# Kernel optimization log

Hardware: AMD Instinct MI355X
Metric: run time of the kernel (lower is better)

The kernel has to match this reference:

```python
import jax, jax.numpy as jnp
import numpy as np

NUM_HEADS = 32
NUM_KV_HEADS = 8
HEAD_DIM = 128
ROPE_BASE = 10000.0


def _rope_tables(seq_len, head_dim, dtype):
    inv_freq = 1.0 / (ROPE_BASE ** (jnp.arange(0, head_dim, 2, dtype=jnp.float32) / head_dim))
    t = jnp.arange(seq_len, dtype=jnp.float32)
    freqs = jnp.einsum('i,j->ij', t, inv_freq)          # [S, D/2]
    emb = jnp.concatenate([freqs, freqs], axis=-1)      # [S, D]
    return jnp.cos(emb).astype(dtype), jnp.sin(emb).astype(dtype)


def _rotate_half(x):
    x1, x2 = jnp.split(x, 2, axis=-1)
    return jnp.concatenate([-x2, x1], axis=-1)


def _apply_rope(x, cos, sin):
    # x: [B, H, S, D]; cos/sin: [S, D] broadcast over batch and heads
    return x * cos[None, None, :, :] + _rotate_half(x) * sin[None, None, :, :]


def setup_inputs() -> dict:
    key = jax.random.key(0)
    k1, k2, k3, k4, k5 = jax.random.split(key, 5)
    B, S, H = 1, 2048, 4096
    scale = 0.02
    return {
        'hidden_states': jax.random.normal(k1, (B, S, H), dtype=jnp.float32),
        'Wq': jax.random.normal(k2, (4096, 4096), dtype=jnp.float32) * scale,
        'Wk': jax.random.normal(k3, (1024, 4096), dtype=jnp.float32) * scale,
        'Wv': jax.random.normal(k4, (1024, 4096), dtype=jnp.float32) * scale,
        'Wo': jax.random.normal(k5, (4096, 4096), dtype=jnp.float32) * scale,
    }


def reference(hidden_states, Wq, Wk, Wv, Wo):
    B, S, hidden = hidden_states.shape
    n_rep = NUM_HEADS // NUM_KV_HEADS

    # projections (torch Linear: y = x @ W.T)
    q = (hidden_states @ Wq.T).reshape(B, S, NUM_HEADS, HEAD_DIM).transpose(0, 2, 1, 3)
    k = (hidden_states @ Wk.T).reshape(B, S, NUM_KV_HEADS, HEAD_DIM).transpose(0, 2, 1, 3)
    v = (hidden_states @ Wv.T).reshape(B, S, NUM_KV_HEADS, HEAD_DIM).transpose(0, 2, 1, 3)

    # RoPE: init path with no past -> query/key position ids both arange(S)
    cos, sin = _rope_tables(S, HEAD_DIM, hidden_states.dtype)
    q = _apply_rope(q, cos, sin)
    k = _apply_rope(k, cos, sin)

    # repeat_kv: [B, Hkv, S, D] -> [B, H, S, D]
    k = jnp.repeat(k, n_rep, axis=1)
    v = jnp.repeat(v, n_rep, axis=1)

    # manual attention with causal mask
    scores = jnp.einsum('bhqd,bhkd->bhqk', q, k) / jnp.sqrt(jnp.float32(HEAD_DIM)).astype(q.dtype)
    causal = jnp.tril(jnp.ones((S, S), dtype=bool))
    scores = jnp.where(causal[None, None, :, :], scores, jnp.finfo(scores.dtype).min)
    probs = jax.nn.softmax(scores, axis=-1)

    out = jnp.einsum('bhqk,bhkd->bhqd', probs, v)        # [B, H, S, D]
    out = out.transpose(0, 2, 1, 3).reshape(B, S, hidden)
    return out @ Wo.T
```

## Files before the change

kernel.cpp:

```cpp
#include <hip/hip_runtime.h>
#include <hip/hip_bf16.h>

typedef __attribute__((ext_vector_type(4))) float f32x4;
typedef __attribute__((ext_vector_type(8))) short short8;
typedef __attribute__((ext_vector_type(4))) unsigned int u32x4;

__device__ __forceinline__ unsigned short f2bf(float f) {
  union { float f; unsigned int u; } v; v.f = f;
  unsigned int r = (v.u + 0x7fffu + ((v.u >> 16) & 1u)) >> 16;
  return (unsigned short)r;
}
__device__ __forceinline__ unsigned short f2bf_fast(float f) {
  __hip_bfloat16 h = __float2bfloat16(f);
  return __builtin_bit_cast(unsigned short, h);
}
__device__ __forceinline__ float bf2f(unsigned short h) {
  union { unsigned int u; float f; } v; v.u = ((unsigned int)h) << 16;
  return v.f;
}
__device__ __forceinline__ unsigned int cvt_pk_bf16(float lo, float hi) {
  unsigned int r;
  asm("v_cvt_pk_bf16_f32 %0, %1, %2" : "=v"(r) : "v"(lo), "v"(hi));
  return r;
}

__device__ __forceinline__ void gload_lds16(const void* g, void* l) {
  __builtin_amdgcn_global_load_lds((const __attribute__((address_space(1))) void*)g,
                                   (__attribute__((address_space(3))) void*)l,
                                   16, 0, 0);
}

template <int N>
__device__ __forceinline__ void vmwait() {
  asm volatile("s_waitcnt vmcnt(%0)" :: "n"(N) : "memory");
}

__global__ __launch_bounds__(256) void cvt_all(
    const float* __restrict__ hid, const float* __restrict__ wq,
    const float* __restrict__ wk, const float* __restrict__ wv,
    const float* __restrict__ wo, unsigned short* __restrict__ out) {
  const size_t E0 = 8388608, E1 = 25165824, E2 = 29360128, E3 = 33554432, E4 = 50331648;
  size_t stride = (size_t)gridDim.x * blockDim.x;
  for (size_t i = (size_t)blockIdx.x * blockDim.x + threadIdx.x; i * 4 < E4; i += stride) {
    size_t i4 = i * 4;
    const float* src; size_t rel;
    if (i4 < E0)      { src = hid; rel = i4; }
    else if (i4 < E1) { src = wq;  rel = i4 - E0; }
    else if (i4 < E2) { src = wk;  rel = i4 - E1; }
    else if (i4 < E3) { src = wv;  rel = i4 - E2; }
    else              { src = wo;  rel = i4 - E3; }
    float4 v = *(const float4*)(src + rel);
    ushort4 o;
    o.x = f2bf(v.x); o.y = f2bf(v.y); o.z = f2bf(v.z); o.w = f2bf(v.w);
    *(ushort4*)(out + i4) = o;
  }
}

template <int BM, int BN, int DEPTH, bool BF16_OUT>
__global__ __launch_bounds__(256, 2) void gemm_p(
    const unsigned short* __restrict__ A,
    const unsigned short* __restrict__ B,
    void* __restrict__ Cout, int M, int N, int K) {
  constexpr int BK = 32;
  constexpr int MFRAG = BM / 32;
  constexpr int NFRAG = BN / 32;
  constexpr int ASHORTS = BM * BK;
  constexpr int BSHORTS = BN * BK;
  constexpr int BUFSH = ASHORTS + BSHORTS;
  constexpr int ALOADS = BM / 64;
  constexpr int BLOADS = BN / 64;
  constexpr int LPT = ALOADS + BLOADS;
  __shared__ unsigned short lds[DEPTH * BUFSH];

  const int tid = threadIdx.x;
  const int wave = tid >> 6, lane = tid & 63;
  const int l15 = lane & 15, l4 = lane >> 4;
  const int row0 = blockIdx.y * BM, col0 = blockIdx.x * BN;
  const int mrow0 = (wave >> 1) * (BM / 2);
  const int ncol0 = (wave & 1) * (BN / 2);
  const int NT = K >> 5;
  const int srow = tid >> 2;
  const int scel = (tid & 3) * 8;

  f32x4 zv = {0.f, 0.f, 0.f, 0.f};
  f32x4 acc[MFRAG][NFRAG];
#pragma unroll
  for (int m = 0; m < MFRAG; ++m)
#pragma unroll
    for (int n = 0; n < NFRAG; ++n) acc[m][n] = zv;

  auto stage = [&](int t) {
    unsigned short* buf = &lds[(t % DEPTH) * BUFSH];
    const int k0 = t * BK;
#pragma unroll
    for (int i = 0; i < ALOADS; ++i)
      gload_lds16(A + (size_t)(row0 + i * 64 + srow) * K + k0 + scel,
                  buf + i * 2048 + tid * 8);
#pragma unroll
    for (int i = 0; i < BLOADS; ++i)
      gload_lds16(B + (size_t)(col0 + i * 64 + srow) * K + k0 + scel,
                  buf + ASHORTS + i * 2048 + tid * 8);
  };

#pragma unroll
  for (int i = 0; i < DEPTH - 1; ++i) stage(i);

  for (int t = 0; t < NT; ++t) {
    const int rem = NT - 1 - t;
    if (rem >= 2)      vmwait<2 * LPT>();
    else if (rem == 1) vmwait<LPT>();
    else               vmwait<0>();
    __builtin_amdgcn_sched_barrier(0);
    __builtin_amdgcn_s_barrier();
    __builtin_amdgcn_sched_barrier(0);
    if (t + DEPTH - 1 < NT) stage(t + DEPTH - 1);

    const unsigned short* Abuf = &lds[(t % DEPTH) * BUFSH];
    const unsigned short* Bbuf = Abuf + ASHORTS;
    short8 bfr[NFRAG], afr[MFRAG];
#pragma unroll
    for (int n = 0; n < NFRAG; ++n)
      bfr[n] = *(const short8*)&Bbuf[(ncol0 + n * 16 + l15) * BK + l4 * 8];
#pragma unroll
    for (int m = 0; m < MFRAG; ++m)
      afr[m] = *(const short8*)&Abuf[(mrow0 + m * 16 + l15) * BK + l4 * 8];
    __builtin_amdgcn_s_setprio(1);
#pragma unroll
    for (int m = 0; m < MFRAG; ++m)
#pragma unroll
      for (int n = 0; n < NFRAG; ++n)
        acc[m][n] = __builtin_amdgcn_mfma_f32_16x16x32_bf16(afr[m], bfr[n], acc[m][n], 0, 0, 0);
    __builtin_amdgcn_s_setprio(0);
    __builtin_amdgcn_sched_barrier(0);
  }

#pragma unroll
  for (int m = 0; m < MFRAG; ++m)
#pragma unroll
    for (int n = 0; n < NFRAG; ++n)
#pragma unroll
      for (int j = 0; j < 4; ++j) {
        int r = row0 + mrow0 + m * 16 + l4 * 4 + j;
        int cc = col0 + ncol0 + n * 16 + l15;
        if constexpr (BF16_OUT)
          ((unsigned short*)Cout)[(size_t)r * N + cc] = f2bf(acc[m][n][j]);
        else
          ((float*)Cout)[(size_t)r * N + cc] = acc[m][n][j];
      }
}

__global__ __launch_bounds__(256) void rope_k(unsigned short* __restrict__ QKV) {
  int idx = blockIdx.x * blockDim.x + threadIdx.x;
  if (idx >= 2048 * 40 * 64) return;
  int j = idx & 63;
  int rest = idx >> 6;
  int slot = rest % 40;
  int s = rest / 40;
  int doff = (slot < 32) ? slot * 128 : 4096 + (slot - 32) * 128;
  unsigned short* p = QKV + (size_t)s * 6144 + doff;
  float inv = exp2f((float)j * -0.20762050593046015f);
  float ang = (float)s * inv;
  float sn, cs;
  sincosf(ang, &sn, &cs);
  float x1 = bf2f(p[j]), x2 = bf2f(p[j + 64]);
  p[j]      = f2bf(x1 * cs - x2 * sn);
  p[j + 64] = f2bf(x2 * cs + x1 * sn);
}

__global__ __launch_bounds__(512, 4) void attn_k(
    const unsigned short* __restrict__ QKV,
    unsigned short* __restrict__ O) {
  __shared__ unsigned short Ks[2][64 * 128];
  __shared__ unsigned short Vs[2][64 * 128];

  const int tid = threadIdx.x;
  const int wave = tid >> 6, lane = tid & 63;
  const int l15 = lane & 15, l4 = lane >> 4;

  const int bid = blockIdx.x;
  const int qt16 = bid & 15;
  const int h = (bid >> 4) & 31;
  const int qt = (h < 16) ? (15 - qt16) : qt16;
  const int hkv = h >> 2;
  const int q0 = qt * 128;
  const int qrow = q0 + wave * 16 + l15;
  const float C2 = 0.12751744219938793f;

  const unsigned short* Qp = QKV + h * 128;
  const unsigned short* Kp = QKV + 4096 + hkv * 128;
  const unsigned short* Vp = QKV + 5120 + hkv * 128;

  const int vpr = tid >> 4;
  const int vd8 = tid & 15;
  const int vg8 = vpr >> 2, vjj = 2 * (vpr & 3);
  const int vn = vd8 >> 1, vch = (vd8 & 1) * 8;

  short8 qf[4];
#pragma unroll
  for (int kc = 0; kc < 4; ++kc)
    qf[kc] = *(const short8*)(Qp + (size_t)qrow * 6144 + kc * 32 + l4 * 8);

  f32x4 zv = {0.f, 0.f, 0.f, 0.f};
  f32x4 oacc[8];
#pragma unroll
  for (int n = 0; n < 8; ++n) oacc[n] = zv;
  float mrow = -3.0e38f, lrow = 0.f;

  auto stageK = [&](int kvn, int b) {
#pragma unroll
    for (int i = 0; i < 2; ++i) {
      int c = wave * 2 + i;
      int row = c * 4 + l4;
      int colel = (l15 * 8) ^ ((row & 7) << 3);
      gload_lds16(Kp + (size_t)(kvn + row) * 6144 + colel, &Ks[b][c * 512]);
    }
  };
  auto loadV = [&](int kvn, short8& va, short8& vb) {
    va = *(const short8*)(Vp + (size_t)(kvn + 2 * vpr) * 6144 + vd8 * 8);
    vb = *(const short8*)(Vp + (size_t)(kvn + 2 * vpr + 1) * 6144 + vd8 * 8);
  };
  auto writeV = [&](int b, const short8& va, const short8& vb) {
#pragma unroll
    for (int i = 0; i < 8; ++i) {
      int c = vch + i;
      unsigned int pack = (unsigned int)(unsigned short)va[i] |
                          ((unsigned int)(unsigned short)vb[i] << 16);
      *(unsigned int*)&Vs[b][vg8 * 1024 + vn * 128 + ((c ^ vn) & 15) * 8 + vjj] = pack;
    }
  };

  {
    short8 va, vb;
    stageK(0, 0);
    loadV(0, va, vb);
    writeV(0, va, vb);
  }
  __syncthreads();

  const int nt = 2 * qt + 2;
  for (int t = 0; t < nt; ++t) {
    const int cur = t & 1, nxt = cur ^ 1;
    const int kv0 = t * 64;
    const bool has_next = (t + 1 < nt);
    short8 va, vb;
    if (has_next) {
      stageK(kv0 + 64, nxt);
      loadV(kv0 + 64, va, vb);
    }

    f32x4 sacc[4];
#pragma unroll
    for (int cb = 0; cb < 4; ++cb) sacc[cb] = zv;
    __builtin_amdgcn_s_setprio(1);
#pragma unroll
    for (int cb = 0; cb < 4; ++cb) {
      int row = cb * 16 + l15;
      int sw = (row & 7) << 3;
#pragma unroll
      for (int kc = 0; kc < 4; ++kc) {
        short8 kf = *(const short8*)&Ks[cur][row * 128 + ((kc * 32 + l4 * 8) ^ sw)];
        sacc[cb] = __builtin_amdgcn_mfma_f32_16x16x32_bf16(kf, qf[kc], sacc[cb], 0, 0, 0);
      }
    }
    __builtin_amdgcn_s_setprio(0);

    if (kv0 + 63 > q0 + wave * 16) {
#pragma unroll
      for (int cb = 0; cb < 4; ++cb)
#pragma unroll
        for (int j = 0; j < 4; ++j) {
          int kvpos = kv0 + cb * 16 + l4 * 4 + j;
          if (kvpos > qrow) sacc[cb][j] = -3.0e38f;
        }
    }

    float pm = sacc[0][0];
#pragma unroll
    for (int cb = 0; cb < 4; ++cb)
#pragma unroll
      for (int j = 0; j < 4; ++j) pm = fmaxf(pm, sacc[cb][j]);
    pm = fmaxf(pm, __shfl_xor(pm, 16, 64));
    pm = fmaxf(pm, __shfl_xor(pm, 32, 64));

    if (__any(pm > mrow + 64.0f)) {
      float mn = fmaxf(mrow, pm);
      float rs = exp2f((mrow - mn) * C2);
      mrow = mn;
      lrow *= rs;
      float rs0 = __shfl(rs, 4 * l4 + 0, 64);
      float rs1 = __shfl(rs, 4 * l4 + 1, 64);
      float rs2 = __shfl(rs, 4 * l4 + 2, 64);
      float rs3 = __shfl(rs, 4 * l4 + 3, 64);
#pragma unroll
      for (int n = 0; n < 8; ++n) {
        oacc[n][0] *= rs0; oacc[n][1] *= rs1;
        oacc[n][2] *= rs2; oacc[n][3] *= rs3;
      }
    }

    unsigned int pack[8];
    float psum = 0.f;
#pragma unroll
    for (int cb = 0; cb < 4; ++cb) {
      float p0 = exp2f((sacc[cb][0] - mrow) * C2);
      float p1 = exp2f((sacc[cb][1] - mrow) * C2);
      float p2 = exp2f((sacc[cb][2] - mrow) * C2);
      float p3 = exp2f((sacc[cb][3] - mrow) * C2);
      psum += (p0 + p1) + (p2 + p3);
      pack[cb * 2 + 0] = cvt_pk_bf16(p0, p1);
      pack[cb * 2 + 1] = cvt_pk_bf16(p2, p3);
    }
    lrow += psum;

#pragma unroll
    for (int ks = 0; ks < 2; ++ks) {
      u32x4 pw;
#pragma unroll
      for (int w = 0; w < 4; ++w) {
        int sl = l15 + 16 * ((2 * l4 + (w >> 1)) & 3);
        int v0 = __shfl((int)pack[4 * ks + (w & 1)], sl, 64);
        int v1 = __shfl((int)pack[4 * ks + 2 + (w & 1)], sl, 64);
        pw[w] = (lane < 32) ? (unsigned int)v0 : (unsigned int)v1;
      }
      short8 pf = __builtin_bit_cast(short8, pw);
      __builtin_amdgcn_s_setprio(1);
#pragma unroll
      for (int n = 0; n < 8; ++n) {
        short8 vf = *(const short8*)&Vs[cur][(ks * 4 + l4) * 1024 + n * 128 + ((l15 ^ n) & 15) * 8];
        oacc[n] = __builtin_amdgcn_mfma_f32_16x16x32_bf16(pf, vf, oacc[n], 0, 0, 0);
      }
      __builtin_amdgcn_s_setprio(0);
    }

    if (has_next) writeV(nxt, va, vb);
    __syncthreads();
  }

  lrow += __shfl_xor(lrow, 16, 64);
  lrow += __shfl_xor(lrow, 32, 64);
  float linv = 1.0f / lrow;
  float li0 = __shfl(linv, 4 * l4 + 0, 64);
  float li1 = __shfl(linv, 4 * l4 + 1, 64);
  float li2 = __shfl(linv, 4 * l4 + 2, 64);
  float li3 = __shfl(linv, 4 * l4 + 3, 64);
#pragma unroll
  for (int n = 0; n < 8; ++n) {
    int r = q0 + wave * 16 + l4 * 4;
    size_t base = (size_t)r * 4096 + h * 128 + n * 16 + l15;
    O[base]          = f2bf_fast(oacc[n][0] * li0);
    O[base + 4096]   = f2bf_fast(oacc[n][1] * li1);
    O[base + 8192]   = f2bf_fast(oacc[n][2] * li2);
    O[base + 12288]  = f2bf_fast(oacc[n][3] * li3);
  }
}

extern "C" void kernel_launch(void* const* d_in, const int* in_sizes, int n_in,
                              void* d_out, int out_size, void* d_ws, size_t ws_size,
                              hipStream_t stream) {
  const float* hid = (const float*)d_in[0];
  const float* Wq  = (const float*)d_in[1];
  const float* Wk  = (const float*)d_in[2];
  const float* Wv  = (const float*)d_in[3];
  const float* Wo  = (const float*)d_in[4];

  char* ws = (char*)d_ws;
  size_t off = 0;
  unsigned short* hid_b = (unsigned short*)(ws + off); off += (size_t)2048 * 4096 * 2;
  unsigned short* Wq_b  = (unsigned short*)(ws + off); off += (size_t)4096 * 4096 * 2;
  unsigned short* Wk_b  = (unsigned short*)(ws + off); off += (size_t)1024 * 4096 * 2;
  unsigned short* Wv_b  = (unsigned short*)(ws + off); off += (size_t)1024 * 4096 * 2;
  unsigned short* Wo_b  = (unsigned short*)(ws + off); off += (size_t)4096 * 4096 * 2;
  unsigned short* QKV   = (unsigned short*)(ws + off); off += (size_t)2048 * 6144 * 2;
  unsigned short* Ob    = (unsigned short*)(ws + off); off += (size_t)2048 * 4096 * 2;
  (void)Wk_b; (void)Wv_b;

  cvt_all<<<4096, 256, 0, stream>>>(hid, Wq, Wk, Wv, Wo, hid_b);

  gemm_p<128, 192, 4, true><<<dim3(32, 16), 256, 0, stream>>>(hid_b, Wq_b, (void*)QKV, 2048, 6144, 4096);

  rope_k<<<20480, 256, 0, stream>>>(QKV);

  attn_k<<<512, 512, 0, stream>>>(QKV, Ob);

  gemm_p<128, 128, 4, false><<<dim3(32, 16), 256, 0, stream>>>(Ob, Wo_b, d_out, 2048, 4096, 4096);
}
```

Baseline: 336.7 us.

## Use BK=64 double-buffered GEMM with XOR-swizzled LDS layout

```diff
diff --git a/kernel.cpp b/kernel.cpp
--- a/kernel.cpp
+++ b/kernel.cpp
@@ -56,21 +56,20 @@
   }
 }
 
-template <int BM, int BN, int DEPTH, bool BF16_OUT>
-__global__ __launch_bounds__(256, 2) void gemm_p(
+template <int BM, int BN, bool BF16_OUT>
+__global__ __launch_bounds__(256, 2) void gemm_p2(
     const unsigned short* __restrict__ A,
     const unsigned short* __restrict__ B,
     void* __restrict__ Cout, int M, int N, int K) {
-  constexpr int BK = 32;
+  constexpr int BK = 64;
   constexpr int MFRAG = BM / 32;
   constexpr int NFRAG = BN / 32;
-  constexpr int ASHORTS = BM * BK;
-  constexpr int BSHORTS = BN * BK;
-  constexpr int BUFSH = ASHORTS + BSHORTS;
-  constexpr int ALOADS = BM / 64;
-  constexpr int BLOADS = BN / 64;
-  constexpr int LPT = ALOADS + BLOADS;
-  __shared__ unsigned short lds[DEPTH * BUFSH];
+  constexpr int ASH = BM * BK;
+  constexpr int BSH = BN * BK;
+  constexpr int BUF = ASH + BSH;
+  constexpr int ALOADS = BM / 32;
+  constexpr int BLOADS = BN / 32;
+  __shared__ unsigned short lds[2 * BUF];
 
   const int tid = threadIdx.x;
   const int wave = tid >> 6, lane = tid & 63;
@@ -78,9 +77,9 @@
   const int row0 = blockIdx.y * BM, col0 = blockIdx.x * BN;
   const int mrow0 = (wave >> 1) * (BM / 2);
   const int ncol0 = (wave & 1) * (BN / 2);
-  const int NT = K >> 5;
-  const int srow = tid >> 2;
-  const int scel = (tid & 3) * 8;
+  const int NT = K >> 6;
+  const int srow = tid >> 3;
+  const int scol = ((tid & 7) ^ (srow & 7)) * 8;
 
   f32x4 zv = {0.f, 0.f, 0.f, 0.f};
   f32x4 acc[MFRAG][NFRAG];
@@ -90,47 +89,50 @@
     for (int n = 0; n < NFRAG; ++n) acc[m][n] = zv;
 
   auto stage = [&](int t) {
-    unsigned short* buf = &lds[(t % DEPTH) * BUFSH];
+    unsigned short* buf = &lds[(t & 1) * BUF];
     const int k0 = t * BK;
 #pragma unroll
     for (int i = 0; i < ALOADS; ++i)
-      gload_lds16(A + (size_t)(row0 + i * 64 + srow) * K + k0 + scel,
+      gload_lds16(A + (size_t)(row0 + i * 32 + srow) * K + k0 + scol,
                   buf + i * 2048 + tid * 8);
 #pragma unroll
     for (int i = 0; i < BLOADS; ++i)
-      gload_lds16(B + (size_t)(col0 + i * 64 + srow) * K + k0 + scel,
-                  buf + ASHORTS + i * 2048 + tid * 8);
+      gload_lds16(B + (size_t)(col0 + i * 32 + srow) * K + k0 + scol,
+                  buf + ASH + i * 2048 + tid * 8);
   };
 
-#pragma unroll
-  for (int i = 0; i < DEPTH - 1; ++i) stage(i);
+  stage(0);
 
   for (int t = 0; t < NT; ++t) {
-    const int rem = NT - 1 - t;
-    if (rem >= 2)      vmwait<2 * LPT>();
-    else if (rem == 1) vmwait<LPT>();
-    else               vmwait<0>();
+    vmwait<0>();
     __builtin_amdgcn_sched_barrier(0);
     __builtin_amdgcn_s_barrier();
     __builtin_amdgcn_sched_barrier(0);
-    if (t + DEPTH - 1 < NT) stage(t + DEPTH - 1);
-
-    const unsigned short* Abuf = &lds[(t % DEPTH) * BUFSH];
-    const unsigned short* Bbuf = Abuf + ASHORTS;
-    short8 bfr[NFRAG], afr[MFRAG];
-#pragma unroll
-    for (int n = 0; n < NFRAG; ++n)
-      bfr[n] = *(const short8*)&Bbuf[(ncol0 + n * 16 + l15) * BK + l4 * 8];
-#pragma unroll
-    for (int m = 0; m < MFRAG; ++m)
-      afr[m] = *(const short8*)&Abuf[(mrow0 + m * 16 + l15) * BK + l4 * 8];
-    __builtin_amdgcn_s_setprio(1);
-#pragma unroll
-    for (int m = 0; m < MFRAG; ++m)
-#pragma unroll
-      for (int n = 0; n < NFRAG; ++n)
-        acc[m][n] = __builtin_amdgcn_mfma_f32_16x16x32_bf16(afr[m], bfr[n], acc[m][n], 0, 0, 0);
-    __builtin_amdgcn_s_setprio(0);
+    if (t + 1 < NT) stage(t + 1);
+
+    const unsigned short* Ab = &lds[(t & 1) * BUF];
+    const unsigned short* Bb = Ab + ASH;
+#pragma unroll
+    for (int h = 0; h < 2; ++h) {
+      short8 afr[MFRAG], bfr[NFRAG];
+#pragma unroll
+      for (int m = 0; m < MFRAG; ++m) {
+        int row = mrow0 + m * 16 + l15;
+        afr[m] = *(const short8*)&Ab[row * 64 + (((h * 4 + l4) ^ (l15 & 7)) * 8)];
+      }
+#pragma unroll
+      for (int n = 0; n < NFRAG; ++n) {
+        int row = ncol0 + n * 16 + l15;
+        bfr[n] = *(const short8*)&Bb[row * 64 + (((h * 4 + l4) ^ (l15 & 7)) * 8)];
+      }
+      __builtin_amdgcn_s_setprio(1);
+#pragma unroll
+      for (int m = 0; m < MFRAG; ++m)
+#pragma unroll
+        for (int n = 0; n < NFRAG; ++n)
+          acc[m][n] = __builtin_amdgcn_mfma_f32_16x16x32_bf16(afr[m], bfr[n], acc[m][n], 0, 0, 0);
+      __builtin_amdgcn_s_setprio(0);
+    }
     __builtin_amdgcn_sched_barrier(0);
   }
 
@@ -376,11 +378,11 @@
 
   cvt_all<<<4096, 256, 0, stream>>>(hid, Wq, Wk, Wv, Wo, hid_b);
 
-  gemm_p<128, 192, 4, true><<<dim3(32, 16), 256, 0, stream>>>(hid_b, Wq_b, (void*)QKV, 2048, 6144, 4096);
+  gemm_p2<128, 192, true><<<dim3(32, 16), 256, 0, stream>>>(hid_b, Wq_b, (void*)QKV, 2048, 6144, 4096);
 
   rope_k<<<20480, 256, 0, stream>>>(QKV);
 
   attn_k<<<512, 512, 0, stream>>>(QKV, Ob);
 
-  gemm_p<128, 128, 4, false><<<dim3(32, 16), 256, 0, stream>>>(Ob, Wo_b, d_out, 2048, 4096, 4096);
-}
+  gemm_p2<128, 128, false><<<dim3(32, 16), 256, 0, stream>>>(Ob, Wo_b, d_out, 2048, 4096, 4096);
+}
```

Measured after the change: 317.2 us. 1.06x faster.
